# Kernel tuning notes

Measured on AMD Instinct MI355X. Metric: run time of the kernel, lower is better.

The kernel has to match this reference:

```python
import jax, jax.numpy as jnp
import numpy as np

N_NODES = 40000
N_EDGES = 640000
D = 128
BN_EPS = 1e-5


def setup_inputs() -> dict:
    key = jax.random.key(0)
    ks = jax.random.split(key, 8)
    h = jax.random.normal(ks[0], (N_NODES, D), dtype=jnp.float32)
    snorm_n = jax.random.uniform(ks[1], (N_NODES, 1), dtype=jnp.float32)
    W_self = jax.random.normal(ks[2], (D, D), dtype=jnp.float32) * 0.05
    W_neigh = jax.random.normal(ks[3], (D, D), dtype=jnp.float32) * 0.05
    b = jax.random.normal(ks[4], (D,), dtype=jnp.float32) * 0.05
    gamma = jnp.ones((D,), dtype=jnp.float32)
    beta = jnp.zeros((D,), dtype=jnp.float32)
    src = jax.random.randint(ks[5], (N_EDGES,), 0, N_NODES, dtype=jnp.int32)
    dst = jax.random.randint(ks[6], (N_EDGES,), 0, N_NODES, dtype=jnp.int32)
    return {"h": h, "snorm_n": snorm_n, "W_self": W_self, "W_neigh": W_neigh,
            "b": b, "gamma": gamma, "beta": beta, "src": src, "dst": dst}


def reference(h, snorm_n, W_self, W_neigh, b, gamma, beta, src, dst):
    h_in = h
    # --- SAGEConv (mean aggregator): mean over in-neighbors (src -> dst) ---
    msg = h[src]                                   # [E, D] irregular gather
    agg = jax.ops.segment_sum(msg, dst, num_segments=N_NODES)  # [N, D]
    deg = jax.ops.segment_sum(jnp.ones((N_EDGES,), h.dtype), dst,
                              num_segments=N_NODES)            # [N]
    h_neigh = agg / jnp.maximum(deg, 1.0)[:, None]
    out = h @ W_self + h_neigh @ W_neigh + b       # fc_self + fc_neigh + bias
    out = jax.nn.relu(out)                         # activation
    # --- graph norm ---
    out = out * snorm_n
    # --- batch norm (training-style batch statistics over nodes) ---
    mean = jnp.mean(out, axis=0)
    var = jnp.var(out, axis=0)
    out = (out - mean) * jax.lax.rsqrt(var + BN_EPS) * gamma + beta
    # --- residual ---
    return h_in + out
```

## Files before the change

kernel.cpp:

```cpp
#include <hip/hip_runtime.h>
#include <hip/hip_bf16.h>

constexpr int N_NODES = 40000;
constexpr int N_EDGES = 640000;
constexpr int D = 128;
constexpr float BN_EPS = 1e-5f;
constexpr int CAP = 128;
constexpr int NTILES = 1250;

typedef __attribute__((ext_vector_type(8))) short short8;
typedef __attribute__((ext_vector_type(4))) float f32x4;

static_assert(N_EDGES == N_NODES * D / 8, "cvt_fill fusion assumes equal ranges");

__device__ __forceinline__ unsigned bf16_rne(float f) {
    unsigned b = __float_as_uint(f);
    return (b + 0x7FFFu + ((b >> 16) & 1u)) >> 16;
}
__device__ __forceinline__ float bflo(unsigned w) { return __uint_as_float(w << 16); }
__device__ __forceinline__ float bfhi(unsigned w) { return __uint_as_float(w & 0xFFFF0000u); }

__global__ void cvt_fill_kernel(const int* __restrict__ dst,
                                const int* __restrict__ src,
                                int* __restrict__ cursor,
                                int* __restrict__ esrc,
                                const float4* __restrict__ h4,
                                uint4* __restrict__ hb4,
                                const float* __restrict__ Wself,
                                const float* __restrict__ Wneigh,
                                uint4* __restrict__ wfrag) {
    int e = blockIdx.x * blockDim.x + threadIdx.x;
    if (e >= N_EDGES) return;
    int t = dst[e];
    int p = atomicAdd(&cursor[t], 1);
    if (p < CAP) esrc[t * CAP + p] = src[e];
    float4 a = h4[2 * e];
    float4 b = h4[2 * e + 1];
    uint4 o;
    o.x = bf16_rne(a.x) | (bf16_rne(a.y) << 16);
    o.y = bf16_rne(a.z) | (bf16_rne(a.w) << 16);
    o.z = bf16_rne(b.x) | (bf16_rne(b.y) << 16);
    o.w = bf16_rne(b.z) | (bf16_rne(b.w) << 16);
    hb4[e] = o;
    if (e < 4096) {
        int G = e;
        int l = G & 63;
        int tile = G >> 6;
        int kg = l >> 4, n = l & 15;
        int ct = tile >> 3, kt = tile & 7;
        int k0 = kt * 32 + kg * 8;
        int col = ct * 16 + n;
        unsigned w[8];
        #pragma unroll
        for (int j = 0; j < 8; j++) {
            int k = k0 + j;
            float v = (k < D) ? Wself[(size_t)k * D + col]
                              : Wneigh[(size_t)(k - D) * D + col];
            w[j] = bf16_rne(v);
        }
        uint4 ow;
        ow.x = w[0] | (w[1] << 16);
        ow.y = w[2] | (w[3] << 16);
        ow.z = w[4] | (w[5] << 16);
        ow.w = w[6] | (w[7] << 16);
        wfrag[G] = ow;
    }
}

__global__ __launch_bounds__(256) void gather_kernel(
        const uint4* __restrict__ hb4,
        const int* __restrict__ cursor,
        const int* __restrict__ esrc,
        uint4* __restrict__ hnb4) {
    int node = (blockIdx.x * blockDim.x + threadIdx.x) >> 6;
    int lane = threadIdx.x & 63;
    if (node >= N_NODES) return;
    int g  = lane & 15;
    int es = lane >> 4;
    int deg = cursor[node];
    int cnt = deg < CAP ? deg : CAP;
    const int* bucket = esrc + node * CAP;
    float acc[8] = {0.f, 0.f, 0.f, 0.f, 0.f, 0.f, 0.f, 0.f};
    for (int j = es; j < cnt; j += 4) {
        int a = bucket[j];
        uint4 v = hb4[(size_t)a * 16 + g];
        acc[0] += bflo(v.x); acc[1] += bfhi(v.x);
        acc[2] += bflo(v.y); acc[3] += bfhi(v.y);
        acc[4] += bflo(v.z); acc[5] += bfhi(v.z);
        acc[6] += bflo(v.w); acc[7] += bfhi(v.w);
    }
    #pragma unroll
    for (int i = 0; i < 8; i++) {
        acc[i] += __shfl_xor(acc[i], 16);
        acc[i] += __shfl_xor(acc[i], 32);
    }
    if (es == 0) {
        float rd = 1.0f / (float)(deg > 1 ? deg : 1);
        uint4 o;
        o.x = bf16_rne(acc[0] * rd) | (bf16_rne(acc[1] * rd) << 16);
        o.y = bf16_rne(acc[2] * rd) | (bf16_rne(acc[3] * rd) << 16);
        o.z = bf16_rne(acc[4] * rd) | (bf16_rne(acc[5] * rd) << 16);
        o.w = bf16_rne(acc[6] * rd) | (bf16_rne(acc[7] * rd) << 16);
        hnb4[(size_t)node * 16 + g] = o;
    }
}

__global__ __launch_bounds__(256) void gemm_kernel(
        const uint4* __restrict__ hb4,
        const uint4* __restrict__ hnb4,
        const uint4* __restrict__ wfrag,
        const float* __restrict__ snorm,
        const float* __restrict__ bias,
        float* __restrict__ pre,
        float* __restrict__ sums,
        float* __restrict__ sumsq) {
    __shared__ uint4 ldsW[2048];
    __shared__ float sums_l[64];
    __shared__ float sumsq_l[64];

    int t = threadIdx.x;
    int lane = t & 63;
    int wid = t >> 6;
    int n = lane & 15;
    int kg = lane >> 4;
    int rowtile = blockIdx.x >> 1;
    int cbt = blockIdx.x & 1;
    int cb = cbt * 64;
    int row_base = rowtile * 64 + wid * 16;
    int row = row_base + n;

    if (t < 64) { sums_l[t] = 0.f; sumsq_l[t] = 0.f; }

    short8 a[8];
    #pragma unroll
    for (int kt = 0; kt < 4; kt++) {
        uint4 v = hb4[(size_t)row * 16 + kt * 4 + kg];
        a[kt] = __builtin_bit_cast(short8, v);
    }
    #pragma unroll
    for (int kt = 0; kt < 4; kt++) {
        uint4 v = hnb4[(size_t)row * 16 + kt * 4 + kg];
        a[4 + kt] = __builtin_bit_cast(short8, v);
    }

    #pragma unroll
    for (int i = 0; i < 8; i++) {
        int g = i * 256 + t;
        ldsW[g] = wfrag[cbt * 2048 + g];
    }
    __syncthreads();

    f32x4 acc[4];
    #pragma unroll
    for (int lt = 0; lt < 4; lt++) acc[lt] = (f32x4){0.f, 0.f, 0.f, 0.f};
    #pragma unroll
    for (int lt = 0; lt < 4; lt++) {
        #pragma unroll
        for (int kt = 0; kt < 8; kt++) {
            short8 b = __builtin_bit_cast(short8, ldsW[(lt * 8 + kt) * 64 + lane]);
            acc[lt] = __builtin_amdgcn_mfma_f32_16x16x32_bf16(a[kt], b, acc[lt], 0, 0, 0);
        }
    }

    float snv[4];
    #pragma unroll
    for (int r = 0; r < 4; r++) snv[r] = snorm[row_base + kg * 4 + r];

    #pragma unroll
    for (int lt = 0; lt < 4; lt++) {
        int col = cb + lt * 16 + n;
        float bb = bias[col];
        float csum = 0.f, csq = 0.f;
        #pragma unroll
        for (int r = 0; r < 4; r++) {
            int rr = row_base + kg * 4 + r;
            float v = acc[lt][r] + bb;
            v = fmaxf(v, 0.f);
            v *= snv[r];
            pre[(size_t)rr * D + col] = v;
            csum += v;
            csq += v * v;
        }
        csum += __shfl_xor(csum, 16); csq += __shfl_xor(csq, 16);
        csum += __shfl_xor(csum, 32); csq += __shfl_xor(csq, 32);
        if (kg == 0) {
            atomicAdd(&sums_l[lt * 16 + n], csum);
            atomicAdd(&sumsq_l[lt * 16 + n], csq);
        }
    }
    __syncthreads();
    if (t < 64) {
        atomicAdd(&sums[cb + t], sums_l[t]);
        atomicAdd(&sumsq[cb + t], sumsq_l[t]);
    }
}

__global__ void final_kernel(const float4* __restrict__ h4,
                             const float4* __restrict__ sums4,
                             const float4* __restrict__ sumsq4,
                             const float4* __restrict__ gamma4,
                             const float4* __restrict__ beta4,
                             float4* __restrict__ out4) {
    int idx = blockIdx.x * blockDim.x + threadIdx.x;
    int total = N_NODES * D / 4;
    if (idx >= total) return;
    int d4 = idx & 31;
    float4 s  = sums4[d4];
    float4 sq = sumsq4[d4];
    float4 g  = gamma4[d4];
    float4 bt = beta4[d4];
    const float invN = 1.0f / (float)N_NODES;
    float4 hv = h4[idx];
    float4 ov = out4[idx];
    float m, var, sc;
    m = s.x * invN; var = sq.x * invN - m * m; sc = g.x * rsqrtf(var + BN_EPS);
    ov.x = hv.x + (ov.x - m) * sc + bt.x;
    m = s.y * invN; var = sq.y * invN - m * m; sc = g.y * rsqrtf(var + BN_EPS);
    ov.y = hv.y + (ov.y - m) * sc + bt.y;
    m = s.z * invN; var = sq.z * invN - m * m; sc = g.z * rsqrtf(var + BN_EPS);
    ov.z = hv.z + (ov.z - m) * sc + bt.z;
    m = s.w * invN; var = sq.w * invN - m * m; sc = g.w * rsqrtf(var + BN_EPS);
    ov.w = hv.w + (ov.w - m) * sc + bt.w;
    out4[idx] = ov;
}

extern "C" void kernel_launch(void* const* d_in, const int* in_sizes, int n_in,
                              void* d_out, int out_size, void* d_ws, size_t ws_size,
                              hipStream_t stream) {
    const float* h      = (const float*)d_in[0];
    const float* snorm  = (const float*)d_in[1];
    const float* Wself  = (const float*)d_in[2];
    const float* Wneigh = (const float*)d_in[3];
    const float* bias   = (const float*)d_in[4];
    const float* gamma  = (const float*)d_in[5];
    const float* beta   = (const float*)d_in[6];
    const int*   src    = (const int*)d_in[7];
    const int*   dst    = (const int*)d_in[8];
    float* out = (float*)d_out;

    int*   cursor = (int*)d_ws;
    float* sums   = (float*)(cursor + N_NODES);
    float* sumsq  = sums + D;
    int*   esrc   = (int*)(sumsq + D);
    size_t off    = (size_t)((char*)(esrc + (size_t)N_NODES * CAP) - (char*)d_ws);
    off = (off + 15) & ~(size_t)15;
    uint4* wfrag = (uint4*)((char*)d_ws + off);
    uint4* hb4   = wfrag + 4096;
    uint4* hnb4  = hb4 + N_NODES * (D / 8);

    size_t zero_bytes = (size_t)(N_NODES + 2 * D) * sizeof(float);
    hipMemsetAsync(d_ws, 0, zero_bytes, stream);

    cvt_fill_kernel<<<N_EDGES / 256, 256, 0, stream>>>(
        dst, src, cursor, esrc, (const float4*)h, hb4, Wself, Wneigh, wfrag);
    gather_kernel<<<N_NODES / 4, 256, 0, stream>>>(hb4, cursor, esrc, hnb4);
    gemm_kernel<<<NTILES, 256, 0, stream>>>(hb4, hnb4, wfrag, snorm, bias,
                                            out, sums, sumsq);
    final_kernel<<<(N_NODES * D / 4) / 256, 256, 0, stream>>>(
        (const float4*)h, (const float4*)sums, (const float4*)sumsq,
        (const float4*)gamma, (const float4*)beta, (float4*)out);
}
```

Measured before the change: 177.5 us.

## Partition CSR fill and gather by destination color to keep buckets XCD-local

Edge bucketing is split out of the per-edge conversion into a grid-strided loop. Each block, chosen by blockIdx mod 8, handles only edges whose destination lies in one eighth of the node range. The gather kernel is remapped so blocks of the same color process that same node range. The aim is that, with blocks dispatched round-robin across XCDs, atomics, esrc writes and the later gather reads stay in one XCD's L2. The cost is that every color group scans the whole dst array, so dst reads grow eightfold, and the fill kernel now loops over edges.

```diff
diff --git a/kernel.cpp b/kernel.cpp
--- a/kernel.cpp
+++ b/kernel.cpp
@@ -7,11 +7,13 @@
 constexpr float BN_EPS = 1e-5f;
 constexpr int CAP = 128;
 constexpr int NTILES = 1250;
+constexpr int NCOLOR = 8;
+constexpr int NODES_PER_COLOR = N_NODES / NCOLOR;
+constexpr int FILL_BLOCKS = 2560;
+constexpr int COLOR_STRIDE = (FILL_BLOCKS / NCOLOR) * 256;
 
 typedef __attribute__((ext_vector_type(8))) short short8;
 typedef __attribute__((ext_vector_type(4))) float f32x4;
-
-static_assert(N_EDGES == N_NODES * D / 8, "cvt_fill fusion assumes equal ranges");
 
 __device__ __forceinline__ unsigned bf16_rne(float f) {
     unsigned b = __float_as_uint(f);
@@ -20,30 +22,30 @@
 __device__ __forceinline__ float bflo(unsigned w) { return __uint_as_float(w << 16); }
 __device__ __forceinline__ float bfhi(unsigned w) { return __uint_as_float(w & 0xFFFF0000u); }
 
-__global__ void cvt_fill_kernel(const int* __restrict__ dst,
-                                const int* __restrict__ src,
-                                int* __restrict__ cursor,
-                                int* __restrict__ esrc,
-                                const float4* __restrict__ h4,
-                                uint4* __restrict__ hb4,
-                                const float* __restrict__ Wself,
-                                const float* __restrict__ Wneigh,
-                                uint4* __restrict__ wfrag) {
-    int e = blockIdx.x * blockDim.x + threadIdx.x;
-    if (e >= N_EDGES) return;
-    int t = dst[e];
-    int p = atomicAdd(&cursor[t], 1);
-    if (p < CAP) esrc[t * CAP + p] = src[e];
-    float4 a = h4[2 * e];
-    float4 b = h4[2 * e + 1];
-    uint4 o;
-    o.x = bf16_rne(a.x) | (bf16_rne(a.y) << 16);
-    o.y = bf16_rne(a.z) | (bf16_rne(a.w) << 16);
-    o.z = bf16_rne(b.x) | (bf16_rne(b.y) << 16);
-    o.w = bf16_rne(b.z) | (bf16_rne(b.w) << 16);
-    hb4[e] = o;
-    if (e < 4096) {
-        int G = e;
+__global__ __launch_bounds__(256) void cvt_fill_kernel(
+        const int* __restrict__ dst,
+        const int* __restrict__ src,
+        int* __restrict__ cursor,
+        int* __restrict__ esrc,
+        const float4* __restrict__ h4,
+        uint4* __restrict__ hb4,
+        const float* __restrict__ Wself,
+        const float* __restrict__ Wneigh,
+        uint4* __restrict__ wfrag) {
+    int gid = blockIdx.x * blockDim.x + threadIdx.x;
+
+    if (gid < N_EDGES) {
+        float4 a = h4[2 * gid];
+        float4 b = h4[2 * gid + 1];
+        uint4 o;
+        o.x = bf16_rne(a.x) | (bf16_rne(a.y) << 16);
+        o.y = bf16_rne(a.z) | (bf16_rne(a.w) << 16);
+        o.z = bf16_rne(b.x) | (bf16_rne(b.y) << 16);
+        o.w = bf16_rne(b.z) | (bf16_rne(b.w) << 16);
+        hb4[gid] = o;
+    }
+    if (gid < 4096) {
+        int G = gid;
         int l = G & 63;
         int tile = G >> 6;
         int kg = l >> 4, n = l & 15;
@@ -65,6 +67,19 @@
         ow.w = w[6] | (w[7] << 16);
         wfrag[G] = ow;
     }
+
+    int c = blockIdx.x & (NCOLOR - 1);
+    int lo = c * NODES_PER_COLOR;
+    int hi = lo + NODES_PER_COLOR;
+    int base = (blockIdx.x >> 3) * 256 + threadIdx.x;
+    for (int e = base; e < N_EDGES; e += COLOR_STRIDE) {
+        int t = dst[e];
+        if (t >= lo && t < hi) {
+            int s = src[e];
+            int p = atomicAdd(&cursor[t], 1);
+            if (p < CAP) esrc[t * CAP + p] = s;
+        }
+    }
 }
 
 __global__ __launch_bounds__(256) void gather_kernel(
@@ -72,9 +87,11 @@
         const int* __restrict__ cursor,
         const int* __restrict__ esrc,
         uint4* __restrict__ hnb4) {
-    int node = (blockIdx.x * blockDim.x + threadIdx.x) >> 6;
+    int c = blockIdx.x & (NCOLOR - 1);
+    int rank = blockIdx.x >> 3;
+    int wid = threadIdx.x >> 6;
+    int node = c * NODES_PER_COLOR + rank * 4 + wid;
     int lane = threadIdx.x & 63;
-    if (node >= N_NODES) return;
     int g  = lane & 15;
     int es = lane >> 4;
     int deg = cursor[node];
@@ -251,7 +268,7 @@
     size_t zero_bytes = (size_t)(N_NODES + 2 * D) * sizeof(float);
     hipMemsetAsync(d_ws, 0, zero_bytes, stream);
 
-    cvt_fill_kernel<<<N_EDGES / 256, 256, 0, stream>>>(
+    cvt_fill_kernel<<<FILL_BLOCKS, 256, 0, stream>>>(
         dst, src, cursor, esrc, (const float4*)h, hb4, Wself, Wneigh, wfrag);
     gather_kernel<<<N_NODES / 4, 256, 0, stream>>>(hb4, cursor, esrc, hnb4);
     gemm_kernel<<<NTILES, 256, 0, stream>>>(hb4, hnb4, wfrag, snorm, bias,
```

Result: no change. 176.6 us (-0.5%).
